# Kernel optimization log

Measured on AMD Instinct MI355X. Metric: run time of the kernel, lower is better.

## Reference

```python
import jax, jax.numpy as jnp
import numpy as np

N_NODES = 100000
N_EDGES = 1600000
D_IN = 128
D_OUT = 128


def setup_inputs() -> dict:
    key = jax.random.key(0)
    k1, k2, k3, k4, k5 = jax.random.split(key, 5)
    H = jax.random.normal(k1, (N_NODES, D_IN), dtype=jnp.float32)
    vals = jax.random.uniform(k2, (N_EDGES,), dtype=jnp.float32)
    W = jax.random.normal(k3, (D_OUT, D_IN), dtype=jnp.float32) * (1.0 / np.sqrt(D_IN))
    rows = jax.random.randint(k4, (N_EDGES,), 0, N_NODES, dtype=jnp.int32)
    cols = jax.random.randint(k5, (N_EDGES,), 0, N_NODES, dtype=jnp.int32)
    return {"H": H, "vals": vals, "W": W, "rows": rows, "cols": cols}


def reference(H, vals, W, rows, cols):
    # Single-rank: communicate_fgm is a no-op (X is zeros, no remote peers).
    # SpMM: out[i] = sum_e vals[e] * H[cols[e]] for edges with rows[e] == i
    msgs = vals[:, None] * H[cols]                      # [n_edges, d_in] irregular gather
    AH = jax.ops.segment_sum(msgs, rows, num_segments=N_NODES)  # [n_nodes, d_in]
    # Linear (no bias) + ReLU
    out = jax.nn.relu(AH @ W.T)                          # [n_nodes, d_out]
    return out
```

## Files before the change

kernel.cpp:

```cpp
#include <hip/hip_runtime.h>

#define N_NODES 100000
#define N_EDGES 1600000
#define D 128
#define CAPR 48
#define NTILES 6250

#define NSUP 196
#define SLOTA 8960
#define CHUNKA 3200
#define NBLKA 500

#define WB_OFF    0u
#define HWB_OFF   65536u
#define SCNTA_OFF 25665536u
#define RCNT_OFF  25669632u
#define RSLOT_OFF 26075136u

typedef unsigned int uint;
typedef __attribute__((ext_vector_type(4))) float f32x4;
typedef __attribute__((ext_vector_type(4))) uint  u32x4;
typedef __attribute__((ext_vector_type(2))) uint  u32x2;
typedef __attribute__((ext_vector_type(2))) int   i32x2;
typedef __attribute__((ext_vector_type(8))) short bf16x8;

__device__ __forceinline__ unsigned short f2bf(float x) {
    uint u = __float_as_uint(x);
    uint r = u + 0x7fffu + ((u >> 16) & 1u);
    return (unsigned short)(r >> 16);
}

__device__ __forceinline__ void acc8(float acc[8], u32x4 q, float v) {
    acc[0] = fmaf(v, __uint_as_float(q.x << 16),         acc[0]);
    acc[1] = fmaf(v, __uint_as_float(q.x & 0xffff0000u), acc[1]);
    acc[2] = fmaf(v, __uint_as_float(q.y << 16),         acc[2]);
    acc[3] = fmaf(v, __uint_as_float(q.y & 0xffff0000u), acc[3]);
    acc[4] = fmaf(v, __uint_as_float(q.z << 16),         acc[4]);
    acc[5] = fmaf(v, __uint_as_float(q.z & 0xffff0000u), acc[5]);
    acc[6] = fmaf(v, __uint_as_float(q.w << 16),         acc[6]);
    acc[7] = fmaf(v, __uint_as_float(q.w & 0xffff0000u), acc[7]);
}

__global__ void k_cast_zero(const float* __restrict__ W, unsigned short* __restrict__ Wb,
                            int* __restrict__ scntA) {
    int b = blockIdx.x;
    if (b < 64) {
        int i = b * 256 + threadIdx.x;
        Wb[i] = f2bf(W[i]);
    } else {
        if (threadIdx.x < NSUP) scntA[threadIdx.x] = 0;
    }
}

__global__ __launch_bounds__(256) void k_gemm_T(const float* __restrict__ H,
                                                const unsigned short* __restrict__ Wb,
                                                unsigned short* __restrict__ HWb) {
    const int wave = threadIdx.x >> 6;
    const int lane = threadIdx.x & 63;
    const int rowtile = blockIdx.x * 4 + wave;
    if (rowtile >= NTILES) return;
    const int rowbase = rowtile * 16;
    const int m    = lane & 15;
    const int quad = lane >> 4;

    f32x4 acc[8];
    #pragma unroll
    for (int nt = 0; nt < 8; ++nt) acc[nt] = (f32x4){0.f, 0.f, 0.f, 0.f};

    const float* hrow = H + (size_t)(rowbase + m) * D;

    #pragma unroll
    for (int ks = 0; ks < 4; ++ks) {
        const int k0 = ks * 32 + quad * 8;
        f32x4 a0 = __builtin_nontemporal_load((const f32x4*)(hrow + k0));
        f32x4 a1 = __builtin_nontemporal_load((const f32x4*)(hrow + k0 + 4));
        bf16x8 hfr;
        hfr[0] = (short)f2bf(a0.x); hfr[1] = (short)f2bf(a0.y);
        hfr[2] = (short)f2bf(a0.z); hfr[3] = (short)f2bf(a0.w);
        hfr[4] = (short)f2bf(a1.x); hfr[5] = (short)f2bf(a1.y);
        hfr[6] = (short)f2bf(a1.z); hfr[7] = (short)f2bf(a1.w);
        #pragma unroll
        for (int nt = 0; nt < 8; ++nt) {
            bf16x8 wfr = *(const bf16x8*)(Wb + (size_t)(nt * 16 + m) * D + k0);
            acc[nt] = __builtin_amdgcn_mfma_f32_16x16x32_bf16(wfr, hfr, acc[nt], 0, 0, 0);
        }
    }

    unsigned short* orow = HWb + (size_t)(rowbase + m) * D;
    #pragma unroll
    for (int nt = 0; nt < 8; ++nt) {
        u32x2 o;
        o.x = (uint)f2bf(acc[nt][0]) | ((uint)f2bf(acc[nt][1]) << 16);
        o.y = (uint)f2bf(acc[nt][2]) | ((uint)f2bf(acc[nt][3]) << 16);
        *(u32x2*)(orow + nt * 16 + quad * 4) = o;
    }
}

__global__ __launch_bounds__(256) void k_bucketA(const int* __restrict__ rows,
                                                 const int* __restrict__ cols,
                                                 const float* __restrict__ vals,
                                                 int* __restrict__ scntA,
                                                 i32x2* __restrict__ epackA) {
    __shared__ int hist[NSUP];
    __shared__ int cur[NSUP];
    const int tid = threadIdx.x;
    const int e0  = blockIdx.x * CHUNKA;

    if (tid < NSUP) hist[tid] = 0;
    __syncthreads();

    for (int i = tid; i < CHUNKA; i += 256)
        atomicAdd(&hist[rows[e0 + i] >> 9], 1);
    __syncthreads();

    if (tid < NSUP) {
        int c = hist[tid];
        int base = (c > 0) ? atomicAdd(&scntA[tid], c) : 0;
        cur[tid] = tid * SLOTA + base;
    }
    __syncthreads();

    for (int i = tid; i < CHUNKA; i += 256) {
        int r = rows[e0 + i];
        int s = r >> 9;
        int p = atomicAdd(&cur[s], 1);
        if (p < (s + 1) * SLOTA)
            epackA[p] = (i32x2){((r & 511) << 17) | cols[e0 + i],
                                __float_as_int(vals[e0 + i])};
    }
}

__global__ __launch_bounds__(512) void k_place(const int* __restrict__ scntA,
                                               const i32x2* __restrict__ epackA,
                                               int* __restrict__ rcnt,
                                               i32x2* __restrict__ rslot) {
    __shared__ int cnt[512];
    const int tid = threadIdx.x;
    const int s   = blockIdx.x;
    const int n   = min(scntA[s], SLOTA);
    const i32x2* src = epackA + (size_t)s * SLOTA;

    cnt[tid] = 0;
    __syncthreads();

    for (int i = tid; i < n; i += 512) {
        i32x2 e  = src[i];
        int   lr = e.x >> 17;
        int   k  = atomicAdd(&cnt[lr], 1);
        int grow = (s << 9) + lr;
        if (k < CAPR && grow < N_NODES)
            rslot[(size_t)grow * CAPR + k] = (i32x2){e.x & 0x1FFFF, e.y};
    }
    __syncthreads();

    int grow = (s << 9) + tid;
    if (grow < N_NODES) rcnt[grow] = cnt[tid];
}

__global__ __launch_bounds__(256) void k_spmm_rows(const int* __restrict__ rcnt,
                                                   const i32x2* __restrict__ rslot,
                                                   const unsigned short* __restrict__ HWb,
                                                   float* __restrict__ out) {
    __shared__ i32x2 sE[32][CAPR];
    __shared__ int   scnt[32];
    const int tid   = threadIdx.x;
    const int lane  = tid & 15;
    const int group = tid >> 4;
    const int row0  = blockIdx.x * 32;

    #pragma unroll
    for (int rr = 0; rr < 2; ++rr) {
        int lr  = group * 2 + rr;
        int row = row0 + lr;
        int cnt = min(rcnt[row], CAPR);
        if (lane == 0) scnt[lr] = cnt;
        for (int j = lane; j < cnt; j += 16)
            sE[lr][j] = __builtin_nontemporal_load(&rslot[(size_t)row * CAPR + j]);
    }
    __syncthreads();

    #pragma unroll
    for (int rr = 0; rr < 2; ++rr) {
        const int lr  = group * 2 + rr;
        const int row = row0 + lr;
        const int e_  = scnt[lr];

        float acc[8];
        #pragma unroll
        for (int c = 0; c < 8; ++c) acc[c] = 0.f;

        int j = 0;
        for (; j + 3 < e_; j += 4) {
            i32x2 e0 = sE[lr][j],     e1 = sE[lr][j + 1];
            i32x2 e2 = sE[lr][j + 2], e3 = sE[lr][j + 3];
            u32x4 q0 = ((const u32x4*)(HWb + (size_t)e0.x * D))[lane];
            u32x4 q1 = ((const u32x4*)(HWb + (size_t)e1.x * D))[lane];
            u32x4 q2 = ((const u32x4*)(HWb + (size_t)e2.x * D))[lane];
            u32x4 q3 = ((const u32x4*)(HWb + (size_t)e3.x * D))[lane];
            acc8(acc, q0, __int_as_float(e0.y));
            acc8(acc, q1, __int_as_float(e1.y));
            acc8(acc, q2, __int_as_float(e2.y));
            acc8(acc, q3, __int_as_float(e3.y));
        }
        for (; j < e_; ++j) {
            i32x2 e = sE[lr][j];
            u32x4 q = ((const u32x4*)(HWb + (size_t)e.x * D))[lane];
            acc8(acc, q, __int_as_float(e.y));
        }

        f32x4 o0 = (f32x4){fmaxf(acc[0], 0.f), fmaxf(acc[1], 0.f),
                           fmaxf(acc[2], 0.f), fmaxf(acc[3], 0.f)};
        f32x4 o1 = (f32x4){fmaxf(acc[4], 0.f), fmaxf(acc[5], 0.f),
                           fmaxf(acc[6], 0.f), fmaxf(acc[7], 0.f)};
        __builtin_nontemporal_store(o0, &((f32x4*)out)[row * 32 + lane * 2]);
        __builtin_nontemporal_store(o1, &((f32x4*)out)[row * 32 + lane * 2 + 1]);
    }
}

extern "C" void kernel_launch(void* const* d_in, const int* in_sizes, int n_in,
                              void* d_out, int out_size, void* d_ws, size_t ws_size,
                              hipStream_t stream) {
    const float* H    = (const float*)d_in[0];
    const float* vals = (const float*)d_in[1];
    const float* W    = (const float*)d_in[2];
    const int*   rows = (const int*)d_in[3];
    const int*   cols = (const int*)d_in[4];
    float* out = (float*)d_out;

    char* ws = (char*)d_ws;
    unsigned short* Wb    = (unsigned short*)(ws + WB_OFF);
    unsigned short* HWb   = (unsigned short*)(ws + HWB_OFF);
    int*            scntA = (int*)(ws + SCNTA_OFF);
    int*            rcnt  = (int*)(ws + RCNT_OFF);
    i32x2*          rslot = (i32x2*)(ws + RSLOT_OFF);
    i32x2*          epackA = (i32x2*)d_out;

    k_cast_zero<<<65, 256, 0, stream>>>(W, Wb, scntA);

    k_gemm_T<<<(NTILES + 3) / 4, 256, 0, stream>>>(H, Wb, HWb);

    k_bucketA<<<NBLKA, 256, 0, stream>>>(rows, cols, vals, scntA, epackA);
    k_place<<<NSUP, 512, 0, stream>>>(scntA, epackA, rcnt, rslot);

    k_spmm_rows<<<N_NODES / 32, 256, 0, stream>>>(rcnt, rslot, HWb, out);
}
```

Before: 252.3 us.

## Fuse all stages into one cooperative persistent kernel with grid syncs

Replaces the five separate launches (cast, GEMM, bucketing, placement, SpMM) with a single cooperative kernel that separates the stages with grid-wide syncs. Within one phase, GEMM and edge bucketing run concurrently on disjoint block ranges. Placement is split into half-supertile blocks, and SpMM becomes a grid-stride loop that reads edge lists straight from global memory instead of staging them in shared memory. The aim is to cut launch gaps and overlap independent stages. The costs are grid-sync latency, occupancy capped by the cooperative launch, and a separate-kernel fallback path.

```diff
diff --git a/kernel.cpp b/kernel.cpp
--- a/kernel.cpp
+++ b/kernel.cpp
@@ -1,4 +1,7 @@
 #include <hip/hip_runtime.h>
+#include <hip/hip_cooperative_groups.h>
+
+namespace cg = cooperative_groups;
 
 #define N_NODES 100000
 #define N_EDGES 1600000
@@ -6,10 +9,12 @@
 #define CAPR 48
 #define NTILES 6250
 
+#define NTHR 256
+#define NBLKA 320
+#define CHUNKA 5000
 #define NSUP 196
 #define SLOTA 8960
-#define CHUNKA 3200
-#define NBLKA 500
+#define NPLACE (2 * NSUP)
 
 #define WB_OFF    0u
 #define HWB_OFF   65536u
@@ -41,86 +46,77 @@
     acc[7] = fmaf(v, __uint_as_float(q.w & 0xffff0000u), acc[7]);
 }
 
-__global__ void k_cast_zero(const float* __restrict__ W, unsigned short* __restrict__ Wb,
-                            int* __restrict__ scntA) {
-    int b = blockIdx.x;
-    if (b < 64) {
-        int i = b * 256 + threadIdx.x;
-        Wb[i] = f2bf(W[i]);
-    } else {
-        if (threadIdx.x < NSUP) scntA[threadIdx.x] = 0;
-    }
-}
-
-__global__ __launch_bounds__(256) void k_gemm_T(const float* __restrict__ H,
-                                                const unsigned short* __restrict__ Wb,
-                                                unsigned short* __restrict__ HWb) {
-    const int wave = threadIdx.x >> 6;
-    const int lane = threadIdx.x & 63;
-    const int rowtile = blockIdx.x * 4 + wave;
-    if (rowtile >= NTILES) return;
-    const int rowbase = rowtile * 16;
+
+__device__ __forceinline__ void do_cast(int bid, int tid, int nblk,
+                                        const float* W, unsigned short* Wb,
+                                        int* scntA) {
+    for (int idx = bid * NTHR + tid; idx < D * D; idx += nblk * NTHR)
+        Wb[idx] = f2bf(W[idx]);
+    if (bid == 0 && tid < NSUP) scntA[tid] = 0;
+}
+
+__device__ __forceinline__ void do_gemm(int bid, int tid, int G,
+                                        const float* H, const unsigned short* Wb,
+                                        unsigned short* HWb) {
+    const int wave = tid >> 6;
+    const int lane = tid & 63;
     const int m    = lane & 15;
     const int quad = lane >> 4;
-
-    f32x4 acc[8];
-    #pragma unroll
-    for (int nt = 0; nt < 8; ++nt) acc[nt] = (f32x4){0.f, 0.f, 0.f, 0.f};
-
-    const float* hrow = H + (size_t)(rowbase + m) * D;
-
-    #pragma unroll
-    for (int ks = 0; ks < 4; ++ks) {
-        const int k0 = ks * 32 + quad * 8;
-        f32x4 a0 = __builtin_nontemporal_load((const f32x4*)(hrow + k0));
-        f32x4 a1 = __builtin_nontemporal_load((const f32x4*)(hrow + k0 + 4));
-        bf16x8 hfr;
-        hfr[0] = (short)f2bf(a0.x); hfr[1] = (short)f2bf(a0.y);
-        hfr[2] = (short)f2bf(a0.z); hfr[3] = (short)f2bf(a0.w);
-        hfr[4] = (short)f2bf(a1.x); hfr[5] = (short)f2bf(a1.y);
-        hfr[6] = (short)f2bf(a1.z); hfr[7] = (short)f2bf(a1.w);
+    for (int rowtile = bid * 4 + wave; rowtile < NTILES; rowtile += G * 4) {
+        const int rowbase = rowtile * 16;
+        f32x4 acc[8];
+        #pragma unroll
+        for (int nt = 0; nt < 8; ++nt) acc[nt] = (f32x4){0.f, 0.f, 0.f, 0.f};
+
+        const float* hrow = H + (size_t)(rowbase + m) * D;
+        #pragma unroll
+        for (int ks = 0; ks < 4; ++ks) {
+            const int k0 = ks * 32 + quad * 8;
+            f32x4 a0 = __builtin_nontemporal_load((const f32x4*)(hrow + k0));
+            f32x4 a1 = __builtin_nontemporal_load((const f32x4*)(hrow + k0 + 4));
+            bf16x8 hfr;
+            hfr[0] = (short)f2bf(a0.x); hfr[1] = (short)f2bf(a0.y);
+            hfr[2] = (short)f2bf(a0.z); hfr[3] = (short)f2bf(a0.w);
+            hfr[4] = (short)f2bf(a1.x); hfr[5] = (short)f2bf(a1.y);
+            hfr[6] = (short)f2bf(a1.z); hfr[7] = (short)f2bf(a1.w);
+            #pragma unroll
+            for (int nt = 0; nt < 8; ++nt) {
+                bf16x8 wfr = *(const bf16x8*)(Wb + (size_t)(nt * 16 + m) * D + k0);
+                acc[nt] = __builtin_amdgcn_mfma_f32_16x16x32_bf16(wfr, hfr, acc[nt], 0, 0, 0);
+            }
+        }
+
+        unsigned short* orow = HWb + (size_t)(rowbase + m) * D;
         #pragma unroll
         for (int nt = 0; nt < 8; ++nt) {
-            bf16x8 wfr = *(const bf16x8*)(Wb + (size_t)(nt * 16 + m) * D + k0);
-            acc[nt] = __builtin_amdgcn_mfma_f32_16x16x32_bf16(wfr, hfr, acc[nt], 0, 0, 0);
-        }
-    }
-
-    unsigned short* orow = HWb + (size_t)(rowbase + m) * D;
-    #pragma unroll
-    for (int nt = 0; nt < 8; ++nt) {
-        u32x2 o;
-        o.x = (uint)f2bf(acc[nt][0]) | ((uint)f2bf(acc[nt][1]) << 16);
-        o.y = (uint)f2bf(acc[nt][2]) | ((uint)f2bf(acc[nt][3]) << 16);
-        *(u32x2*)(orow + nt * 16 + quad * 4) = o;
-    }
-}
-
-__global__ __launch_bounds__(256) void k_bucketA(const int* __restrict__ rows,
-                                                 const int* __restrict__ cols,
-                                                 const float* __restrict__ vals,
-                                                 int* __restrict__ scntA,
-                                                 i32x2* __restrict__ epackA) {
+            u32x2 o;
+            o.x = (uint)f2bf(acc[nt][0]) | ((uint)f2bf(acc[nt][1]) << 16);
+            o.y = (uint)f2bf(acc[nt][2]) | ((uint)f2bf(acc[nt][3]) << 16);
+            *(u32x2*)(orow + nt * 16 + quad * 4) = o;
+        }
+    }
+}
+
+__device__ __forceinline__ void do_bucketA(int abid, int tid,
+                                           const int* rows, const int* cols,
+                                           const float* vals, int* scntA,
+                                           i32x2* epackA) {
     __shared__ int hist[NSUP];
     __shared__ int cur[NSUP];
-    const int tid = threadIdx.x;
-    const int e0  = blockIdx.x * CHUNKA;
+    const int e0 = abid * CHUNKA;
 
     if (tid < NSUP) hist[tid] = 0;
     __syncthreads();
-
-    for (int i = tid; i < CHUNKA; i += 256)
+    for (int i = tid; i < CHUNKA; i += NTHR)
         atomicAdd(&hist[rows[e0 + i] >> 9], 1);
     __syncthreads();
-
     if (tid < NSUP) {
         int c = hist[tid];
         int base = (c > 0) ? atomicAdd(&scntA[tid], c) : 0;
         cur[tid] = tid * SLOTA + base;
     }
     __syncthreads();
-
-    for (int i = tid; i < CHUNKA; i += 256) {
+    for (int i = tid; i < CHUNKA; i += NTHR) {
         int r = rows[e0 + i];
         int s = r >> 9;
         int p = atomicAdd(&cur[s], 1);
@@ -130,60 +126,38 @@
     }
 }
 
-__global__ __launch_bounds__(512) void k_place(const int* __restrict__ scntA,
-                                               const i32x2* __restrict__ epackA,
-                                               int* __restrict__ rcnt,
-                                               i32x2* __restrict__ rslot) {
-    __shared__ int cnt[512];
-    const int tid = threadIdx.x;
-    const int s   = blockIdx.x;
-    const int n   = min(scntA[s], SLOTA);
+__device__ __forceinline__ void do_place(int pbid, int tid, const int* scntA,
+                                         const i32x2* epackA, int* rcnt,
+                                         i32x2* rslot) {
+    __shared__ int cnt[NTHR];
+    const int s = pbid >> 1;
+    const int h = pbid & 1;
+    const int n = min(scntA[s], SLOTA);
     const i32x2* src = epackA + (size_t)s * SLOTA;
 
     cnt[tid] = 0;
     __syncthreads();
-
-    for (int i = tid; i < n; i += 512) {
+    for (int i = tid; i < n; i += NTHR) {
         i32x2 e  = src[i];
         int   lr = e.x >> 17;
-        int   k  = atomicAdd(&cnt[lr], 1);
-        int grow = (s << 9) + lr;
-        if (k < CAPR && grow < N_NODES)
-            rslot[(size_t)grow * CAPR + k] = (i32x2){e.x & 0x1FFFF, e.y};
-    }
-    __syncthreads();
-
-    int grow = (s << 9) + tid;
-    if (grow < N_NODES) rcnt[grow] = cnt[tid];
-}
-
-__global__ __launch_bounds__(256) void k_spmm_rows(const int* __restrict__ rcnt,
-                                                   const i32x2* __restrict__ rslot,
-                                                   const unsigned short* __restrict__ HWb,
-                                                   float* __restrict__ out) {
-    __shared__ i32x2 sE[32][CAPR];
-    __shared__ int   scnt[32];
-    const int tid   = threadIdx.x;
-    const int lane  = tid & 15;
-    const int group = tid >> 4;
-    const int row0  = blockIdx.x * 32;
-
-    #pragma unroll
-    for (int rr = 0; rr < 2; ++rr) {
-        int lr  = group * 2 + rr;
-        int row = row0 + lr;
-        int cnt = min(rcnt[row], CAPR);
-        if (lane == 0) scnt[lr] = cnt;
-        for (int j = lane; j < cnt; j += 16)
-            sE[lr][j] = __builtin_nontemporal_load(&rslot[(size_t)row * CAPR + j]);
-    }
-    __syncthreads();
-
-    #pragma unroll
-    for (int rr = 0; rr < 2; ++rr) {
-        const int lr  = group * 2 + rr;
-        const int row = row0 + lr;
-        const int e_  = scnt[lr];
+        if ((lr >> 8) == h) {
+            int k = atomicAdd(&cnt[lr & 255], 1);
+            if (k < CAPR)
+                rslot[(size_t)((s << 9) + lr) * CAPR + k] =
+                    (i32x2){e.x & 0x1FFFF, e.y};
+        }
+    }
+    __syncthreads();
+    int grow = (s << 9) + (h << 8) + tid;
+    if (grow < N_NODES) rcnt[grow] = min(cnt[tid], CAPR);
+}
+
+__device__ __forceinline__ void do_spmm(int gid, int gstride, int lane,
+                                        const int* rcnt, const i32x2* rslot,
+                                        const unsigned short* HWb, float* out) {
+    for (int row = gid; row < N_NODES; row += gstride) {
+        const int e_ = rcnt[row];
+        const i32x2* el = rslot + (size_t)row * CAPR;
 
         float acc[8];
         #pragma unroll
@@ -191,8 +165,8 @@
 
         int j = 0;
         for (; j + 3 < e_; j += 4) {
-            i32x2 e0 = sE[lr][j],     e1 = sE[lr][j + 1];
-            i32x2 e2 = sE[lr][j + 2], e3 = sE[lr][j + 3];
+            i32x2 e0 = el[j],     e1 = el[j + 1];
+            i32x2 e2 = el[j + 2], e3 = el[j + 3];
             u32x4 q0 = ((const u32x4*)(HWb + (size_t)e0.x * D))[lane];
             u32x4 q1 = ((const u32x4*)(HWb + (size_t)e1.x * D))[lane];
             u32x4 q2 = ((const u32x4*)(HWb + (size_t)e2.x * D))[lane];
@@ -203,7 +177,7 @@
             acc8(acc, q3, __int_as_float(e3.y));
         }
         for (; j < e_; ++j) {
-            i32x2 e = sE[lr][j];
+            i32x2 e = el[j];
             u32x4 q = ((const u32x4*)(HWb + (size_t)e.x * D))[lane];
             acc8(acc, q, __int_as_float(e.y));
         }
@@ -215,6 +189,63 @@
         __builtin_nontemporal_store(o0, &((f32x4*)out)[row * 32 + lane * 2]);
         __builtin_nontemporal_store(o1, &((f32x4*)out)[row * 32 + lane * 2 + 1]);
     }
+}
+
+__global__ __launch_bounds__(NTHR, 4) void k_fused(
+        const float* __restrict__ H, const float* __restrict__ vals,
+        const float* __restrict__ W, const int* __restrict__ rows,
+        const int* __restrict__ cols, unsigned short* __restrict__ Wb,
+        unsigned short* __restrict__ HWb, int* __restrict__ scntA,
+        int* __restrict__ rcnt, i32x2* __restrict__ rslot,
+        i32x2* epackA, float* out) {
+    cg::grid_group grid = cg::this_grid();
+    const int bid  = blockIdx.x;
+    const int tid  = threadIdx.x;
+    const int nblk = gridDim.x;
+
+    do_cast(bid, tid, nblk, W, Wb, scntA);
+    grid.sync();
+
+    const int G = nblk - NBLKA;
+    if (bid < G) do_gemm(bid, tid, G, H, Wb, HWb);
+    else         do_bucketA(bid - G, tid, rows, cols, vals, scntA, epackA);
+    grid.sync();
+
+    if (bid < NPLACE) do_place(bid, tid, scntA, epackA, rcnt, rslot);
+    grid.sync();
+
+    do_spmm(bid * 16 + (tid >> 4), nblk * 16, tid & 15, rcnt, rslot, HWb, out);
+}
+
+__global__ __launch_bounds__(NTHR) void k_cast(const float* __restrict__ W,
+                                               unsigned short* __restrict__ Wb,
+                                               int* __restrict__ scntA) {
+    do_cast(blockIdx.x, threadIdx.x, 64, W, Wb, scntA);
+}
+__global__ __launch_bounds__(NTHR) void k_gemm(const float* __restrict__ H,
+                                               const unsigned short* __restrict__ Wb,
+                                               unsigned short* __restrict__ HWb) {
+    do_gemm(blockIdx.x, threadIdx.x, 1563, H, Wb, HWb);
+}
+__global__ __launch_bounds__(NTHR) void k_bucketA(const int* __restrict__ rows,
+                                                  const int* __restrict__ cols,
+                                                  const float* __restrict__ vals,
+                                                  int* __restrict__ scntA,
+                                                  i32x2* __restrict__ epackA) {
+    do_bucketA(blockIdx.x, threadIdx.x, rows, cols, vals, scntA, epackA);
+}
+__global__ __launch_bounds__(NTHR) void k_place_f(const int* __restrict__ scntA,
+                                                  const i32x2* __restrict__ epackA,
+                                                  int* __restrict__ rcnt,
+                                                  i32x2* __restrict__ rslot) {
+    do_place(blockIdx.x, threadIdx.x, scntA, epackA, rcnt, rslot);
+}
+__global__ __launch_bounds__(NTHR) void k_spmm(const int* __restrict__ rcnt,
+                                               const i32x2* __restrict__ rslot,
+                                               const unsigned short* __restrict__ HWb,
+                                               float* __restrict__ out) {
+    do_spmm(blockIdx.x * 16 + (threadIdx.x >> 4), 1536 * 16, threadIdx.x & 15,
+            rcnt, rslot, HWb, out);
 }
 
 extern "C" void kernel_launch(void* const* d_in, const int* in_sizes, int n_in,
@@ -228,19 +259,41 @@
     float* out = (float*)d_out;
 
     char* ws = (char*)d_ws;
-    unsigned short* Wb    = (unsigned short*)(ws + WB_OFF);
-    unsigned short* HWb   = (unsigned short*)(ws + HWB_OFF);
-    int*            scntA = (int*)(ws + SCNTA_OFF);
-    int*            rcnt  = (int*)(ws + RCNT_OFF);
-    i32x2*          rslot = (i32x2*)(ws + RSLOT_OFF);
+    unsigned short* Wb     = (unsigned short*)(ws + WB_OFF);
+    unsigned short* HWb    = (unsigned short*)(ws + HWB_OFF);
+    int*            scntA  = (int*)(ws + SCNTA_OFF);
+    int*            rcnt   = (int*)(ws + RCNT_OFF);
+    i32x2*          rslot  = (i32x2*)(ws + RSLOT_OFF);
     i32x2*          epackA = (i32x2*)d_out;
 
-    k_cast_zero<<<65, 256, 0, stream>>>(W, Wb, scntA);
-
-    k_gemm_T<<<(NTILES + 3) / 4, 256, 0, stream>>>(H, Wb, HWb);
-
-    k_bucketA<<<NBLKA, 256, 0, stream>>>(rows, cols, vals, scntA, epackA);
-    k_place<<<NSUP, 512, 0, stream>>>(scntA, epackA, rcnt, rslot);
-
-    k_spmm_rows<<<N_NODES / 32, 256, 0, stream>>>(rcnt, rslot, HWb, out);
-}
+    static int s_nblk = -1;
+    if (s_nblk < 0) {
+        int bpc = 0, ncu = 0;
+        if (hipOccupancyMaxActiveBlocksPerMultiprocessor(
+                &bpc, (const void*)k_fused, NTHR, 0) != hipSuccess || bpc < 1)
+            bpc = 2;
+        if (hipDeviceGetAttribute(&ncu, hipDeviceAttributeMultiprocessorCount, 0)
+                != hipSuccess || ncu < 1)
+            ncu = 256;
+        long t = (long)bpc * ncu;
+        if (t > 2048) t = 2048;
+        if (t < NPLACE + 8) t = NPLACE + 8;
+        s_nblk = (int)t;
+    }
+
+    void* args[12] = {
+        (void*)&H, (void*)&vals, (void*)&W, (void*)&rows, (void*)&cols,
+        (void*)&Wb, (void*)&HWb, (void*)&scntA, (void*)&rcnt, (void*)&rslot,
+        (void*)&epackA, (void*)&out
+    };
+    hipError_t st = hipLaunchCooperativeKernel((const void*)k_fused,
+                                               dim3(s_nblk), dim3(NTHR),
+                                               args, 0, stream);
+    if (st != hipSuccess) {
+        k_cast<<<64, NTHR, 0, stream>>>(W, Wb, scntA);
+        k_gemm<<<1563, NTHR, 0, stream>>>(H, Wb, HWb);
+        k_bucketA<<<NBLKA, NTHR, 0, stream>>>(rows, cols, vals, scntA, epackA);
+        k_place_f<<<NPLACE, NTHR, 0, stream>>>(scntA, epackA, rcnt, rslot);
+        k_spmm<<<1536, NTHR, 0, stream>>>(rcnt, rslot, HWb, out);
+    }
+}
```

New measurement: 458.4 us. +81.7%, slower.

## Fuse GEMM with edge bucketing and fold row placement into SpMM kernel

Applied to the files above, without the earlier changes.

Merges the bf16 GEMM and the first-level edge bucketing into one launch with block-index dispatch, so the two independent stages can run concurrently. It also removes the separate placement kernel and its global per-row slot buffer. Each SpMM block now reads its super-bucket, filters the edges for one quarter into shared memory, and bins them into 32-row groups before gathering. This cuts one launch and the rslot write/read round trip, but each super-bucket is scanned four times and the SpMM blocks carry a large LDS footprint and extra barriers, which may lower occupancy.

```diff
diff --git a/kernel.cpp b/kernel.cpp
--- a/kernel.cpp
+++ b/kernel.cpp
@@ -6,16 +6,20 @@
 #define CAPR 48
 #define NTILES 6250
 
+#define NTHR 256
+#define NBA 640
+#define CHUNKA 2500
+#define NGB 1563
 #define NSUP 196
 #define SLOTA 8960
-#define CHUNKA 3200
-#define NBLKA 500
-
-#define WB_OFF    0u
-#define HWB_OFF   65536u
-#define SCNTA_OFF 25665536u
-#define RCNT_OFF  25669632u
-#define RSLOT_OFF 26075136u
+#define NPS (NSUP * 4)
+#define NTHR3 512
+#define EQCAP 2464
+
+#define WB_OFF     0u
+#define HWB_OFF    65536u
+#define SCNTA_OFF  25665536u
+#define EPACKA_OFF 25669632u
 
 typedef unsigned int uint;
 typedef __attribute__((ext_vector_type(4))) float f32x4;
@@ -41,23 +45,56 @@
     acc[7] = fmaf(v, __uint_as_float(q.w & 0xffff0000u), acc[7]);
 }
 
-__global__ void k_cast_zero(const float* __restrict__ W, unsigned short* __restrict__ Wb,
-                            int* __restrict__ scntA) {
+__global__ __launch_bounds__(NTHR) void k_cast(const float* __restrict__ W,
+                                               unsigned short* __restrict__ Wb,
+                                               int* __restrict__ scntA) {
     int b = blockIdx.x;
     if (b < 64) {
-        int i = b * 256 + threadIdx.x;
+        int i = b * NTHR + threadIdx.x;
         Wb[i] = f2bf(W[i]);
     } else {
         if (threadIdx.x < NSUP) scntA[threadIdx.x] = 0;
     }
 }
 
-__global__ __launch_bounds__(256) void k_gemm_T(const float* __restrict__ H,
-                                                const unsigned short* __restrict__ Wb,
-                                                unsigned short* __restrict__ HWb) {
-    const int wave = threadIdx.x >> 6;
-    const int lane = threadIdx.x & 63;
-    const int rowtile = blockIdx.x * 4 + wave;
+__global__ __launch_bounds__(NTHR) void k_gemm_bucketA(
+        const float* __restrict__ H, const unsigned short* __restrict__ Wb,
+        unsigned short* __restrict__ HWb, const int* __restrict__ rows,
+        const int* __restrict__ cols, const float* __restrict__ vals,
+        int* __restrict__ scntA, i32x2* __restrict__ epackA) {
+    const int bid = blockIdx.x;
+    const int tid = threadIdx.x;
+
+    if (bid < NBA) {
+        __shared__ int hist[NSUP];
+        __shared__ int cur[NSUP];
+        const int e0 = bid * CHUNKA;
+
+        if (tid < NSUP) hist[tid] = 0;
+        __syncthreads();
+        for (int i = tid; i < CHUNKA; i += NTHR)
+            atomicAdd(&hist[rows[e0 + i] >> 9], 1);
+        __syncthreads();
+        if (tid < NSUP) {
+            int c = hist[tid];
+            int base = (c > 0) ? atomicAdd(&scntA[tid], c) : 0;
+            cur[tid] = tid * SLOTA + base;
+        }
+        __syncthreads();
+        for (int i = tid; i < CHUNKA; i += NTHR) {
+            int r = rows[e0 + i];
+            int s = r >> 9;
+            int p = atomicAdd(&cur[s], 1);
+            if (p < (s + 1) * SLOTA)
+                epackA[p] = (i32x2){((r & 511) << 17) | cols[e0 + i],
+                                    __float_as_int(vals[e0 + i])};
+        }
+        return;
+    }
+
+    const int wave = tid >> 6;
+    const int lane = tid & 63;
+    const int rowtile = (bid - NBA) * 4 + wave;
     if (rowtile >= NTILES) return;
     const int rowbase = rowtile * 16;
     const int m    = lane & 15;
@@ -68,7 +105,6 @@
     for (int nt = 0; nt < 8; ++nt) acc[nt] = (f32x4){0.f, 0.f, 0.f, 0.f};
 
     const float* hrow = H + (size_t)(rowbase + m) * D;
-
     #pragma unroll
     for (int ks = 0; ks < 4; ++ks) {
         const int k0 = ks * 32 + quad * 8;
@@ -96,124 +132,85 @@
     }
 }
 
-__global__ __launch_bounds__(256) void k_bucketA(const int* __restrict__ rows,
-                                                 const int* __restrict__ cols,
-                                                 const float* __restrict__ vals,
-                                                 int* __restrict__ scntA,
-                                                 i32x2* __restrict__ epackA) {
-    __shared__ int hist[NSUP];
-    __shared__ int cur[NSUP];
+__global__ __launch_bounds__(NTHR3) void k_spmm_q(const int* __restrict__ scntA,
+                                                  const i32x2* __restrict__ epackA,
+                                                  const unsigned short* __restrict__ HWb,
+                                                  float* __restrict__ out) {
+    __shared__ i32x2 eq[EQCAP];
+    __shared__ i32x2 sE[32][CAPR + 1];
+    __shared__ int   cnt[32];
+    __shared__ int   qcnt;
     const int tid = threadIdx.x;
-    const int e0  = blockIdx.x * CHUNKA;
-
-    if (tid < NSUP) hist[tid] = 0;
-    __syncthreads();
-
-    for (int i = tid; i < CHUNKA; i += 256)
-        atomicAdd(&hist[rows[e0 + i] >> 9], 1);
-    __syncthreads();
-
-    if (tid < NSUP) {
-        int c = hist[tid];
-        int base = (c > 0) ? atomicAdd(&scntA[tid], c) : 0;
-        cur[tid] = tid * SLOTA + base;
-    }
-    __syncthreads();
-
-    for (int i = tid; i < CHUNKA; i += 256) {
-        int r = rows[e0 + i];
-        int s = r >> 9;
-        int p = atomicAdd(&cur[s], 1);
-        if (p < (s + 1) * SLOTA)
-            epackA[p] = (i32x2){((r & 511) << 17) | cols[e0 + i],
-                                __float_as_int(vals[e0 + i])};
-    }
-}
-
-__global__ __launch_bounds__(512) void k_place(const int* __restrict__ scntA,
-                                               const i32x2* __restrict__ epackA,
-                                               int* __restrict__ rcnt,
-                                               i32x2* __restrict__ rslot) {
-    __shared__ int cnt[512];
-    const int tid = threadIdx.x;
-    const int s   = blockIdx.x;
+    const int s   = blockIdx.x >> 2;
+    const int q   = blockIdx.x & 3;
     const int n   = min(scntA[s], SLOTA);
     const i32x2* src = epackA + (size_t)s * SLOTA;
 
-    cnt[tid] = 0;
+    if (tid == 0) qcnt = 0;
     __syncthreads();
-
-    for (int i = tid; i < n; i += 512) {
+    for (int i = tid; i < n; i += NTHR3) {
         i32x2 e  = src[i];
         int   lr = e.x >> 17;
-        int   k  = atomicAdd(&cnt[lr], 1);
-        int grow = (s << 9) + lr;
-        if (k < CAPR && grow < N_NODES)
-            rslot[(size_t)grow * CAPR + k] = (i32x2){e.x & 0x1FFFF, e.y};
+        if ((lr >> 7) == q) {
+            int k = atomicAdd(&qcnt, 1);
+            if (k < EQCAP)
+                eq[k] = (i32x2){((lr & 127) << 17) | (e.x & 0x1FFFF), e.y};
+        }
     }
     __syncthreads();
 
-    int grow = (s << 9) + tid;
-    if (grow < N_NODES) rcnt[grow] = cnt[tid];
-}
-
-__global__ __launch_bounds__(256) void k_spmm_rows(const int* __restrict__ rcnt,
-                                                   const i32x2* __restrict__ rslot,
-                                                   const unsigned short* __restrict__ HWb,
-                                                   float* __restrict__ out) {
-    __shared__ i32x2 sE[32][CAPR];
-    __shared__ int   scnt[32];
-    const int tid   = threadIdx.x;
-    const int lane  = tid & 15;
-    const int group = tid >> 4;
-    const int row0  = blockIdx.x * 32;
-
-    #pragma unroll
-    for (int rr = 0; rr < 2; ++rr) {
-        int lr  = group * 2 + rr;
-        int row = row0 + lr;
-        int cnt = min(rcnt[row], CAPR);
-        if (lane == 0) scnt[lr] = cnt;
-        for (int j = lane; j < cnt; j += 16)
-            sE[lr][j] = __builtin_nontemporal_load(&rslot[(size_t)row * CAPR + j]);
-    }
-    __syncthreads();
-
-    #pragma unroll
-    for (int rr = 0; rr < 2; ++rr) {
-        const int lr  = group * 2 + rr;
-        const int row = row0 + lr;
-        const int e_  = scnt[lr];
-
-        float acc[8];
-        #pragma unroll
-        for (int c = 0; c < 8; ++c) acc[c] = 0.f;
-
-        int j = 0;
-        for (; j + 3 < e_; j += 4) {
-            i32x2 e0 = sE[lr][j],     e1 = sE[lr][j + 1];
-            i32x2 e2 = sE[lr][j + 2], e3 = sE[lr][j + 3];
-            u32x4 q0 = ((const u32x4*)(HWb + (size_t)e0.x * D))[lane];
-            u32x4 q1 = ((const u32x4*)(HWb + (size_t)e1.x * D))[lane];
-            u32x4 q2 = ((const u32x4*)(HWb + (size_t)e2.x * D))[lane];
-            u32x4 q3 = ((const u32x4*)(HWb + (size_t)e3.x * D))[lane];
-            acc8(acc, q0, __int_as_float(e0.y));
-            acc8(acc, q1, __int_as_float(e1.y));
-            acc8(acc, q2, __int_as_float(e2.y));
-            acc8(acc, q3, __int_as_float(e3.y));
-        }
-        for (; j < e_; ++j) {
-            i32x2 e = sE[lr][j];
-            u32x4 q = ((const u32x4*)(HWb + (size_t)e.x * D))[lane];
-            acc8(acc, q, __int_as_float(e.y));
-        }
-
-        f32x4 o0 = (f32x4){fmaxf(acc[0], 0.f), fmaxf(acc[1], 0.f),
-                           fmaxf(acc[2], 0.f), fmaxf(acc[3], 0.f)};
-        f32x4 o1 = (f32x4){fmaxf(acc[4], 0.f), fmaxf(acc[5], 0.f),
-                           fmaxf(acc[6], 0.f), fmaxf(acc[7], 0.f)};
-        __builtin_nontemporal_store(o0, &((f32x4*)out)[row * 32 + lane * 2]);
-        __builtin_nontemporal_store(o1, &((f32x4*)out)[row * 32 + lane * 2 + 1]);
+    const int ne      = min(qcnt, EQCAP);
+    const int rowbase = (s << 9) + (q << 7);
+    const int lane    = tid & 15;
+    const int g       = tid >> 4;
+
+    for (int c = 0; c < 4; ++c) {
+        if (tid < 32) cnt[tid] = 0;
+        __syncthreads();
+        for (int i = tid; i < ne; i += NTHR3) {
+            i32x2 e  = eq[i];
+            int   lr = e.x >> 17;
+            if ((lr >> 5) == c) {
+                int k = atomicAdd(&cnt[lr & 31], 1);
+                if (k < CAPR) sE[lr & 31][k] = (i32x2){e.x & 0x1FFFF, e.y};
+            }
+        }
+        __syncthreads();
+
+        const int row = rowbase + c * 32 + g;
+        if (row < N_NODES) {
+            const int e_ = min(cnt[g], CAPR);
+            float acc[8];
+            #pragma unroll
+            for (int k = 0; k < 8; ++k) acc[k] = 0.f;
+
+            int j = 0;
+            for (; j + 3 < e_; j += 4) {
+                i32x2 e0 = sE[g][j],     e1 = sE[g][j + 1];
+                i32x2 e2 = sE[g][j + 2], e3 = sE[g][j + 3];
+                u32x4 q0 = ((const u32x4*)(HWb + (size_t)e0.x * D))[lane];
+                u32x4 q1 = ((const u32x4*)(HWb + (size_t)e1.x * D))[lane];
+                u32x4 q2 = ((const u32x4*)(HWb + (size_t)e2.x * D))[lane];
+                u32x4 q3 = ((const u32x4*)(HWb + (size_t)e3.x * D))[lane];
+                acc8(acc, q0, __int_as_float(e0.y));
+                acc8(acc, q1, __int_as_float(e1.y));
+                acc8(acc, q2, __int_as_float(e2.y));
+                acc8(acc, q3, __int_as_float(e3.y));
+            }
+            for (; j < e_; ++j) {
+                i32x2 e = sE[g][j];
+                u32x4 qq = ((const u32x4*)(HWb + (size_t)e.x * D))[lane];
+                acc8(acc, qq, __int_as_float(e.y));
+            }
+
+            f32x4 o0 = (f32x4){fmaxf(acc[0], 0.f), fmaxf(acc[1], 0.f),
+                               fmaxf(acc[2], 0.f), fmaxf(acc[3], 0.f)};
+            f32x4 o1 = (f32x4){fmaxf(acc[4], 0.f), fmaxf(acc[5], 0.f),
+                               fmaxf(acc[6], 0.f), fmaxf(acc[7], 0.f)};
+            __builtin_nontemporal_store(o0, &((f32x4*)out)[row * 32 + lane * 2]);
+            __builtin_nontemporal_store(o1, &((f32x4*)out)[row * 32 + lane * 2 + 1]);
+        }
+        __syncthreads();
     }
 }
 
@@ -228,19 +225,15 @@
     float* out = (float*)d_out;
 
     char* ws = (char*)d_ws;
-    unsigned short* Wb    = (unsigned short*)(ws + WB_OFF);
-    unsigned short* HWb   = (unsigned short*)(ws + HWB_OFF);
-    int*            scntA = (int*)(ws + SCNTA_OFF);
-    int*            rcnt  = (int*)(ws + RCNT_OFF);
-    i32x2*          rslot = (i32x2*)(ws + RSLOT_OFF);
-    i32x2*          epackA = (i32x2*)d_out;
-
-    k_cast_zero<<<65, 256, 0, stream>>>(W, Wb, scntA);
-
-    k_gemm_T<<<(NTILES + 3) / 4, 256, 0, stream>>>(H, Wb, HWb);
-
-    k_bucketA<<<NBLKA, 256, 0, stream>>>(rows, cols, vals, scntA, epackA);
-    k_place<<<NSUP, 512, 0, stream>>>(scntA, epackA, rcnt, rslot);
-
-    k_spmm_rows<<<N_NODES / 32, 256, 0, stream>>>(rcnt, rslot, HWb, out);
-}
+    unsigned short* Wb     = (unsigned short*)(ws + WB_OFF);
+    unsigned short* HWb    = (unsigned short*)(ws + HWB_OFF);
+    int*            scntA  = (int*)(ws + SCNTA_OFF);
+    i32x2*          epackA = (i32x2*)(ws + EPACKA_OFF);
+
+    k_cast<<<65, NTHR, 0, stream>>>(W, Wb, scntA);
+
+    k_gemm_bucketA<<<NBA + NGB, NTHR, 0, stream>>>(H, Wb, HWb, rows, cols,
+                                                   vals, scntA, epackA);
+
+    k_spmm_q<<<NPS, NTHR3, 0, stream>>>(scntA, epackA, HWb, out);
+}
```

After: 239.9 us. 4.9% less time.

## Merge cast with bucketing and GEMM with placement into shared launches

Applied to the files above, without the earlier changes.

Replaces the five kernels with a memset plus three launches. The W cast now runs as extra blocks of the bucketing kernel, and the GEMM and the row-placement pass are packed into one grid, with placement split into two half-superblocks of 256 threads each. The goal is to cut launch gaps and let the compute-heavy GEMM overlap the latency-bound scatter placement. The costs are that each placement block scans the whole superblock and discards half the entries, and that bucket chunk sizes changed.

```diff
diff --git a/kernel.cpp b/kernel.cpp
--- a/kernel.cpp
+++ b/kernel.cpp
@@ -6,10 +6,14 @@
 #define CAPR 48
 #define NTILES 6250
 
+#define NTHR 256
+#define NBA 640
+#define CHUNKA 2500
+#define NCAST 64
+#define NGB 1563
 #define NSUP 196
 #define SLOTA 8960
-#define CHUNKA 3200
-#define NBLKA 500
+#define NPLACE (2 * NSUP)
 
 #define WB_OFF    0u
 #define HWB_OFF   65536u
@@ -41,23 +45,82 @@
     acc[7] = fmaf(v, __uint_as_float(q.w & 0xffff0000u), acc[7]);
 }
 
-__global__ void k_cast_zero(const float* __restrict__ W, unsigned short* __restrict__ Wb,
-                            int* __restrict__ scntA) {
-    int b = blockIdx.x;
-    if (b < 64) {
-        int i = b * 256 + threadIdx.x;
+__global__ __launch_bounds__(NTHR) void k_bucketA_cast(
+        const int* __restrict__ rows, const int* __restrict__ cols,
+        const float* __restrict__ vals, int* __restrict__ scntA,
+        i32x2* __restrict__ epackA, const float* __restrict__ W,
+        unsigned short* __restrict__ Wb) {
+    const int bid = blockIdx.x;
+    const int tid = threadIdx.x;
+
+    if (bid >= NBA) {
+        int i = (bid - NBA) * NTHR + tid;
         Wb[i] = f2bf(W[i]);
-    } else {
-        if (threadIdx.x < NSUP) scntA[threadIdx.x] = 0;
-    }
-}
-
-__global__ __launch_bounds__(256) void k_gemm_T(const float* __restrict__ H,
-                                                const unsigned short* __restrict__ Wb,
-                                                unsigned short* __restrict__ HWb) {
-    const int wave = threadIdx.x >> 6;
-    const int lane = threadIdx.x & 63;
-    const int rowtile = blockIdx.x * 4 + wave;
+        return;
+    }
+
+    __shared__ int hist[NSUP];
+    __shared__ int cur[NSUP];
+    const int e0 = bid * CHUNKA;
+
+    if (tid < NSUP) hist[tid] = 0;
+    __syncthreads();
+    for (int i = tid; i < CHUNKA; i += NTHR)
+        atomicAdd(&hist[rows[e0 + i] >> 9], 1);
+    __syncthreads();
+    if (tid < NSUP) {
+        int c = hist[tid];
+        int base = (c > 0) ? atomicAdd(&scntA[tid], c) : 0;
+        cur[tid] = tid * SLOTA + base;
+    }
+    __syncthreads();
+    for (int i = tid; i < CHUNKA; i += NTHR) {
+        int r = rows[e0 + i];
+        int s = r >> 9;
+        int p = atomicAdd(&cur[s], 1);
+        if (p < (s + 1) * SLOTA)
+            epackA[p] = (i32x2){((r & 511) << 17) | cols[e0 + i],
+                                __float_as_int(vals[e0 + i])};
+    }
+}
+
+__global__ __launch_bounds__(NTHR) void k_gemm_place(
+        const float* __restrict__ H, const unsigned short* __restrict__ Wb,
+        unsigned short* __restrict__ HWb, const int* __restrict__ scntA,
+        const i32x2* __restrict__ epackA, int* __restrict__ rcnt,
+        i32x2* __restrict__ rslot) {
+    const int bid = blockIdx.x;
+    const int tid = threadIdx.x;
+
+    if (bid >= NGB) {
+        __shared__ int cnt[NTHR];
+        const int pbid = bid - NGB;
+        const int s = pbid >> 1;
+        const int h = pbid & 1;
+        const int n = min(scntA[s], SLOTA);
+        const i32x2* src = epackA + (size_t)s * SLOTA;
+
+        cnt[tid] = 0;
+        __syncthreads();
+        for (int i = tid; i < n; i += NTHR) {
+            i32x2 e  = src[i];
+            int   lr = e.x >> 17;
+            if ((lr >> 8) == h) {
+                int k = atomicAdd(&cnt[lr & 255], 1);
+                if (k < CAPR)
+                    rslot[(size_t)((s << 9) + lr) * CAPR + k] =
+                        (i32x2){e.x & 0x1FFFF, e.y};
+            }
+        }
+        __syncthreads();
+        int grow = (s << 9) + (h << 8) + tid;
+        if (grow < N_NODES) rcnt[grow] = min(cnt[tid], CAPR);
+        return;
+    }
+
+    const int wave = tid >> 6;
+    const int lane = tid & 63;
+    const int rowtile = bid * 4 + wave;
     if (rowtile >= NTILES) return;
     const int rowbase = rowtile * 16;
     const int m    = lane & 15;
@@ -68,7 +131,6 @@
     for (int nt = 0; nt < 8; ++nt) acc[nt] = (f32x4){0.f, 0.f, 0.f, 0.f};
 
     const float* hrow = H + (size_t)(rowbase + m) * D;
-
     #pragma unroll
     for (int ks = 0; ks < 4; ++ks) {
         const int k0 = ks * 32 + quad * 8;
@@ -96,71 +158,10 @@
     }
 }
 
-__global__ __launch_bounds__(256) void k_bucketA(const int* __restrict__ rows,
-                                                 const int* __restrict__ cols,
-                                                 const float* __restrict__ vals,
-                                                 int* __restrict__ scntA,
-                                                 i32x2* __restrict__ epackA) {
-    __shared__ int hist[NSUP];
-    __shared__ int cur[NSUP];
-    const int tid = threadIdx.x;
-    const int e0  = blockIdx.x * CHUNKA;
-
-    if (tid < NSUP) hist[tid] = 0;
-    __syncthreads();
-
-    for (int i = tid; i < CHUNKA; i += 256)
-        atomicAdd(&hist[rows[e0 + i] >> 9], 1);
-    __syncthreads();
-
-    if (tid < NSUP) {
-        int c = hist[tid];
-        int base = (c > 0) ? atomicAdd(&scntA[tid], c) : 0;
-        cur[tid] = tid * SLOTA + base;
-    }
-    __syncthreads();
-
-    for (int i = tid; i < CHUNKA; i += 256) {
-        int r = rows[e0 + i];
-        int s = r >> 9;
-        int p = atomicAdd(&cur[s], 1);
-        if (p < (s + 1) * SLOTA)
-            epackA[p] = (i32x2){((r & 511) << 17) | cols[e0 + i],
-                                __float_as_int(vals[e0 + i])};
-    }
-}
-
-__global__ __launch_bounds__(512) void k_place(const int* __restrict__ scntA,
-                                               const i32x2* __restrict__ epackA,
-                                               int* __restrict__ rcnt,
-                                               i32x2* __restrict__ rslot) {
-    __shared__ int cnt[512];
-    const int tid = threadIdx.x;
-    const int s   = blockIdx.x;
-    const int n   = min(scntA[s], SLOTA);
-    const i32x2* src = epackA + (size_t)s * SLOTA;
-
-    cnt[tid] = 0;
-    __syncthreads();
-
-    for (int i = tid; i < n; i += 512) {
-        i32x2 e  = src[i];
-        int   lr = e.x >> 17;
-        int   k  = atomicAdd(&cnt[lr], 1);
-        int grow = (s << 9) + lr;
-        if (k < CAPR && grow < N_NODES)
-            rslot[(size_t)grow * CAPR + k] = (i32x2){e.x & 0x1FFFF, e.y};
-    }
-    __syncthreads();
-
-    int grow = (s << 9) + tid;
-    if (grow < N_NODES) rcnt[grow] = cnt[tid];
-}
-
-__global__ __launch_bounds__(256) void k_spmm_rows(const int* __restrict__ rcnt,
-                                                   const i32x2* __restrict__ rslot,
-                                                   const unsigned short* __restrict__ HWb,
-                                                   float* __restrict__ out) {
+__global__ __launch_bounds__(NTHR) void k_spmm_rows(const int* __restrict__ rcnt,
+                                                    const i32x2* __restrict__ rslot,
+                                                    const unsigned short* __restrict__ HWb,
+                                                    float* __restrict__ out) {
     __shared__ i32x2 sE[32][CAPR];
     __shared__ int   scnt[32];
     const int tid   = threadIdx.x;
@@ -228,19 +229,20 @@
     float* out = (float*)d_out;
 
     char* ws = (char*)d_ws;
-    unsigned short* Wb    = (unsigned short*)(ws + WB_OFF);
-    unsigned short* HWb   = (unsigned short*)(ws + HWB_OFF);
-    int*            scntA = (int*)(ws + SCNTA_OFF);
-    int*            rcnt  = (int*)(ws + RCNT_OFF);
-    i32x2*          rslot = (i32x2*)(ws + RSLOT_OFF);
+    unsigned short* Wb     = (unsigned short*)(ws + WB_OFF);
+    unsigned short* HWb    = (unsigned short*)(ws + HWB_OFF);
+    int*            scntA  = (int*)(ws + SCNTA_OFF);
+    int*            rcnt   = (int*)(ws + RCNT_OFF);
+    i32x2*          rslot  = (i32x2*)(ws + RSLOT_OFF);
     i32x2*          epackA = (i32x2*)d_out;
 
-    k_cast_zero<<<65, 256, 0, stream>>>(W, Wb, scntA);
-
-    k_gemm_T<<<(NTILES + 3) / 4, 256, 0, stream>>>(H, Wb, HWb);
-
-    k_bucketA<<<NBLKA, 256, 0, stream>>>(rows, cols, vals, scntA, epackA);
-    k_place<<<NSUP, 512, 0, stream>>>(scntA, epackA, rcnt, rslot);
-
-    k_spmm_rows<<<N_NODES / 32, 256, 0, stream>>>(rcnt, rslot, HWb, out);
-}
+    hipMemsetAsync(scntA, 0, NSUP * sizeof(int), stream);
+
+    k_bucketA_cast<<<NBA + NCAST, NTHR, 0, stream>>>(rows, cols, vals, scntA,
+                                                     epackA, W, Wb);
+
+    k_gemm_place<<<NGB + NPLACE, NTHR, 0, stream>>>(H, Wb, HWb, scntA, epackA,
+                                                    rcnt, rslot);
+
+    k_spmm_rows<<<N_NODES / 32, NTHR, 0, stream>>>(rcnt, rslot, HWb, out);
+}
```

Measured after the change: 251.0 us. No clear change (-0.5%).
